# Kernel optimization log

Measured on AMD Instinct MI355X. Metric: run time of the kernel, lower is better.

The kernel has to match this reference:

```python
import jax, jax.numpy as jnp
import numpy as np

MAX_REL = 64  # max_relative_position
LN_EPS = 1e-5


def _relative_positions(seq_len):
    r = jnp.arange(seq_len)
    rel = jnp.clip(r[None, :] - r[:, None], -MAX_REL, MAX_REL) + MAX_REL
    return rel  # [S, S] int32 in [0, 2*MAX_REL]


def setup_inputs() -> dict:
    key = jax.random.key(0)
    ks = jax.random.split(key, 8)
    B, S, H = 8, 1024, 128
    sd = 1.0 / np.sqrt(H)
    return {
        "x": jax.random.normal(ks[0], (B, S, H), jnp.float32),
        "Wq": jax.random.normal(ks[1], (H, H), jnp.float32) * sd,
        "bq": jnp.zeros((H,), jnp.float32),
        "Wk": jax.random.normal(ks[2], (H, H), jnp.float32) * sd,
        "bk": jnp.zeros((H,), jnp.float32),
        "Wv": jax.random.normal(ks[3], (H, H), jnp.float32) * sd,
        "bv": jnp.zeros((H,), jnp.float32),
        "rel_k": jax.random.normal(ks[4], (2 * MAX_REL + 1, H), jnp.float32),
        "rel_v": jax.random.normal(ks[5], (2 * MAX_REL + 1, H), jnp.float32),
        "Wo": jax.random.normal(ks[6], (H, H), jnp.float32) * sd,
        "bo": jnp.zeros((H,), jnp.float32),
        "gamma": jnp.ones((H,), jnp.float32),
        "beta": jnpp if False else jnp.zeros((H,), jnp.float32),
    }


def reference(x, Wq, bq, Wk, bk, Wv, bv, rel_k, rel_v, Wo, bo, gamma, beta):
    B, S, H = x.shape
    scale = jnp.sqrt(jnp.asarray(H, x.dtype))

    q = x @ Wq + bq  # [B,S,H]
    k = x @ Wk + bk
    v = x @ Wv + bv

    scores = jnp.einsum("bih,bjh->bij", q, k) / scale  # [B,S,S]

    relpos = _relative_positions(S)            # [S,S] int
    rk = rel_k[relpos]                          # [S,S,H] gather
    scores = scores + jnp.einsum("bih,ijh->bij", q, rk)

    attn = jax.nn.softmax(scores, axis=-1)      # dropout = identity (eval)

    ctx = jnp.einsum("bij,bjh->bih", attn, v)
    rv = rel_v[relpos]                          # [S,S,H] gather
    ctx = ctx + jnp.einsum("bij,ijh->bih", attn, rv)

    out = ctx @ Wo + bo

    # residual + LayerNorm
    y = out + x
    mu = jnp.mean(y, axis=-1, keepdims=True)
    var = jnp.mean(jnp.square(y - mu), axis=-1, keepdims=True)
    y = (y - mu) * jax.lax.rsqrt(var + LN_EPS) * gamma + beta
    return y, attn
```

## Files before the change

kernel.cpp:

```cpp
#include <hip/hip_runtime.h>

constexpr int Bn = 8, Sn = 1024, Hn = 128, Rn = 129, RLD = 132;
constexpr float INV_SCALE = 0.088388347648318447f;
constexpr size_t YEL = (size_t)Bn * Sn * Hn;

typedef short bf16x8 __attribute__((ext_vector_type(8)));
typedef short v4s __attribute__((ext_vector_type(4)));
typedef float f32x4 __attribute__((ext_vector_type(4)));
typedef int v4i __attribute__((ext_vector_type(4)));

__device__ __forceinline__ float bf2f(short s) {
    unsigned u = ((unsigned)(unsigned short)s) << 16;
    float f; __builtin_memcpy(&f, &u, 4); return f;
}
__device__ __forceinline__ short f2bf(float f) {
    unsigned u; __builtin_memcpy(&u, &f, 4);
    unsigned r = (u + 0x7fffu + ((u >> 16) & 1u)) >> 16;
    return (short)(r & 0xffffu);
}

__global__ __launch_bounds__(384) void build_relcat(
    const float* __restrict__ rel_k, short* __restrict__ relcat)
{
    const int p = blockIdx.x, c = threadIdx.x;
    const int j = (c < 256) ? (c & 127) : (c - 256);
    float v = rel_k[p * Hn + j];
    short h = f2bf(v);
    relcat[p * 384 + c] = (c < 256) ? h : f2bf(v - bf2f(h));
}

__global__ __launch_bounds__(256) void build_bcat(
    const float* __restrict__ rel_v, const float* __restrict__ Wo,
    short* __restrict__ BcatT)
{
    int idx = blockIdx.x * 256 + threadIdx.x;
    int k = idx >> 7, n = idx & 127;
    float v;
    if (k < 128) v = Wo[k * Hn + n];
    else if (k < 257) {
        int p = k - 128; float a = 0.f;
        for (int h = 0; h < Hn; ++h) a += rel_v[p * Hn + h] * Wo[h * Hn + n];
        v = a;
    } else v = 0.f;
    BcatT[n * 320 + k] = f2bf(v);
}

__global__ __launch_bounds__(256) void proj(
    const float* __restrict__ X,
    const float* __restrict__ Wq, const float* __restrict__ bq,
    const float* __restrict__ Wk, const float* __restrict__ bk,
    const float* __restrict__ Wv, const float* __restrict__ bv,
    short* __restrict__ qh, short* __restrict__ qcat,
    short* __restrict__ kh, short* __restrict__ vT)
{
    __shared__ float xs[64][128];
    __shared__ float wsm[32][128];
    const int tid = threadIdx.x;
    const int sel = blockIdx.y;
    const int row0 = blockIdx.x * 64;
    const float* W = (sel == 0) ? Wq : (sel == 1) ? Wk : Wv;
    const float* bias = (sel == 0) ? bq : (sel == 1) ? bk : bv;

#pragma unroll
    for (int it = 0; it < 8; ++it) {
        int u = tid + it * 256;
        int r = u >> 5, c4 = (u & 31) * 4;
        *(float4*)&xs[r][c4] = *(const float4*)(X + (size_t)(row0 + r) * 128 + c4);
    }

    const int rg = tid >> 5, cg = tid & 31;
    float acc[8][4] = {};
    for (int kc = 0; kc < 128; kc += 32) {
#pragma unroll
        for (int it = 0; it < 4; ++it) {
            int u = tid + it * 256;
            int kk = u >> 5, c4 = (u & 31) * 4;
            *(float4*)&wsm[kk][c4] = *(const float4*)(W + (size_t)(kc + kk) * 128 + c4);
        }
        __syncthreads();
#pragma unroll 8
        for (int kk = 0; kk < 32; ++kk) {
            float wv[4];
#pragma unroll
            for (int c = 0; c < 4; ++c) wv[c] = wsm[kk][cg + c * 32];
#pragma unroll
            for (int r = 0; r < 8; ++r) {
                float xv = xs[rg * 8 + r][kc + kk];
#pragma unroll
                for (int c = 0; c < 4; ++c) acc[r][c] += xv * wv[c];
            }
        }
        __syncthreads();
    }

#pragma unroll
    for (int c = 0; c < 4; ++c) {
        int col = cg + c * 32;
        float bv2 = bias[col];
#pragma unroll
        for (int r = 0; r < 8; ++r) {
            int row = row0 + rg * 8 + r;
            float v = acc[r][c] + bv2;
            short h = f2bf(v);
            if (sel == 0) {
                qh[(size_t)row * 128 + col] = h;
                qcat[(size_t)row * 256 + col] = h;
                qcat[(size_t)row * 256 + 128 + col] = f2bf(v - bf2f(h));
            } else if (sel == 1) {
                kh[(size_t)row * 128 + col] = h;
            } else {
                int b = row >> 10, i = row & (Sn - 1);
                vT[(size_t)b * 131072 + (size_t)col * 1024 + i] = h;
            }
        }
    }
}

__global__ __launch_bounds__(256) void qrel_gemm(
    const short* __restrict__ qcat, const short* __restrict__ relcat,
    float* __restrict__ qrel)
{
    __shared__ short As[64][72];
    __shared__ short Bs[64][72];
    const int tid = threadIdx.x;
    const int wave = tid >> 6, lane = tid & 63;
    const int quad = lane >> 4, l15 = lane & 15;
    const int row0 = blockIdx.x * 64, col0 = blockIdx.y * 64;

    f32x4 acc[4] = {};
    for (int kc = 0; kc < 384; kc += 64) {
#pragma unroll
        for (int it = 0; it < 2; ++it) {
            int u = tid + it * 256;
            int r = u >> 3, c8 = (u & 7) * 8;
            int srcc = kc + c8;
            if (srcc >= 256) srcc -= 256;
            *(v4i*)&As[r][c8] = *(const v4i*)(qcat + (size_t)(row0 + r) * 256 + srcc);
        }
#pragma unroll
        for (int it = 0; it < 2; ++it) {
            int u = tid + it * 256;
            int r = u >> 3, c8 = (u & 7) * 8;
            v4i val = {0, 0, 0, 0};
            if (col0 + r < Rn)
                val = *(const v4i*)(relcat + (size_t)(col0 + r) * 384 + kc + c8);
            *(v4i*)&Bs[r][c8] = val;
        }
        __syncthreads();
#pragma unroll
        for (int ks = 0; ks < 64; ks += 32) {
            bf16x8 af = *(const bf16x8*)&As[wave * 16 + l15][ks + quad * 8];
#pragma unroll
            for (int nt = 0; nt < 4; ++nt) {
                bf16x8 bf = *(const bf16x8*)&Bs[nt * 16 + l15][ks + quad * 8];
                acc[nt] = __builtin_amdgcn_mfma_f32_16x16x32_bf16(af, bf, acc[nt], 0, 0, 0);
            }
        }
        __syncthreads();
    }
    const int rloc0 = wave * 16 + quad * 4;
#pragma unroll
    for (int nt = 0; nt < 4; ++nt) {
        int col = col0 + nt * 16 + l15;
#pragma unroll
        for (int r = 0; r < 4; ++r) {
            if (col < Rn)
                qrel[(size_t)(row0 + rloc0 + r) * RLD + col] = acc[nt][r];
        }
    }
}

__global__ __launch_bounds__(512, 4) void fused_attn(
    const short* __restrict__ qh, const short* __restrict__ kh,
    const short* __restrict__ vT, const float* __restrict__ qrel_g,
    const short* __restrict__ BcatT,
    const float* __restrict__ X, const float* __restrict__ bo,
    const float* __restrict__ gamma, const float* __restrict__ beta,
    float* __restrict__ attn_g, float* __restrict__ y_g)
{
    __shared__ __align__(16) char smem[80896];
    short* KTs  = (short*)smem;
    short* Pb   = (short*)(smem + 34816);
    short* CtxA = (short*)(smem + 67840);
    float* QrL  = (float*)(smem + 67840);
    float* redM = (float*)(smem + 78848);
    float* redS = redM + 128;
    float* redL = redS + 128;
    float* redH = redL + 128;

    const int tid = threadIdx.x;
    const int w = tid >> 6, lane = tid & 63;
    const int quad = lane >> 4, l15 = lane & 15;
    const int bz = blockIdx.z;
    const int row0 = blockIdx.x * 16;
    const size_t grow0 = (size_t)bz * Sn + row0;

#pragma unroll
    for (int rr = 0; rr < 2; ++rr) {
        int r = w * 2 + rr;
        const float* src = qrel_g + (grow0 + r) * RLD;
        QrL[r * 132 + lane] = src[lane];
        QrL[r * 132 + 64 + lane] = src[64 + lane];
        if (lane < 4) QrL[r * 132 + 128 + lane] = src[128 + lane];
    }

    bf16x8 afr[4];
#pragma unroll
    for (int kk = 0; kk < 4; ++kk)
        afr[kk] = *(const bf16x8*)(qh + (grow0 + l15) * 128 + kk * 32 + quad * 8);

    const short* khb = kh + (size_t)bz * Sn * 128;
    f32x4 acc[8] = {};
    for (int kt = 0; kt < 8; ++kt) {
#pragma unroll
        for (int it = 0; it < 4; ++it) {
            int u = tid + it * 512;
            int r = u >> 4, c8 = (u & 15) * 8;
            *(v4i*)&KTs[r * 136 + c8] = *(const v4i*)(khb + (size_t)(kt * 128 + r) * 128 + c8);
        }
        __syncthreads();
#pragma unroll
        for (int kk = 0; kk < 4; ++kk) {
            bf16x8 b = *(const bf16x8*)&KTs[(w * 16 + l15) * 136 + kk * 32 + quad * 8];
            acc[kt] = __builtin_amdgcn_mfma_f32_16x16x32_bf16(afr[kk], b, acc[kt], 0, 0, 0);
        }
        __syncthreads();
    }

    float mx[4];
#pragma unroll
    for (int r = 0; r < 4; ++r) {
        int lr = quad * 4 + r, i = row0 + lr;
        float m = -3.4e38f;
#pragma unroll
        for (int kt = 0; kt < 8; ++kt) {
            int col = kt * 128 + w * 16 + l15;
            int d = col - i; d = (d < -64) ? -64 : (d > 64 ? 64 : d);
            float v = acc[kt][r] * INV_SCALE + QrL[lr * 132 + d + 64];
            acc[kt][r] = v;
            m = fmaxf(m, v);
        }
#pragma unroll
        for (int msk = 1; msk < 16; msk <<= 1) m = fmaxf(m, __shfl_xor(m, msk));
        if (l15 == 0) redM[lr * 8 + w] = m;
    }
    __syncthreads();
#pragma unroll
    for (int r = 0; r < 4; ++r) {
        int lr = quad * 4 + r;
        float m = redM[lr * 8];
#pragma unroll
        for (int j = 1; j < 8; ++j) m = fmaxf(m, redM[lr * 8 + j]);
        mx[r] = m;
    }

#pragma unroll
    for (int r = 0; r < 4; ++r) {
        int lr = quad * 4 + r, i = row0 + lr;
        float s = 0.f, lo = 0.f, hi = 0.f;
#pragma unroll
        for (int kt = 0; kt < 8; ++kt) {
            float e = __expf(acc[kt][r] - mx[r]);
            acc[kt][r] = e;
            s += e;
            int col = kt * 128 + w * 16 + l15;
            lo += (col <= i - 64) ? e : 0.f;
            hi += (col >= i + 64) ? e : 0.f;
        }
#pragma unroll
        for (int msk = 1; msk < 16; msk <<= 1) {
            s += __shfl_xor(s, msk);
            lo += __shfl_xor(lo, msk);
            hi += __shfl_xor(hi, msk);
        }
        if (l15 == 0) { redS[lr * 8 + w] = s; redL[lr * 8 + w] = lo; redH[lr * 8 + w] = hi; }
    }
    __syncthreads();

#pragma unroll
    for (int r = 0; r < 4; ++r) {
        int lr = quad * 4 + r;
        float s = 0.f;
#pragma unroll
        for (int j = 0; j < 8; ++j) s += redS[lr * 8 + j];
        float inv = 1.0f / s;
        float* arow = attn_g + (grow0 + lr) * Sn;
#pragma unroll
        for (int kt = 0; kt < 8; ++kt) {
            int col = kt * 128 + w * 16 + l15;
            float v = acc[kt][r] * inv;
            arow[col] = v;
            Pb[lr * 1032 + col] = f2bf(v);
        }
    }
    __syncthreads();

    const short* vtb = vT + (size_t)bz * 131072;
    f32x4 cacc = {};
    for (int kc = 0; kc < 8; ++kc) {
#pragma unroll
        for (int it = 0; it < 4; ++it) {
            int u = tid + it * 512;
            int r = u >> 4, c8 = (u & 15) * 8;
            *(v4i*)&KTs[r * 136 + c8] = *(const v4i*)(vtb + (size_t)r * 1024 + kc * 128 + c8);
        }
        __syncthreads();
#pragma unroll
        for (int kk = 0; kk < 4; ++kk) {
            bf16x8 a = *(const bf16x8*)&Pb[l15 * 1032 + kc * 128 + kk * 32 + quad * 8];
            bf16x8 b = *(const bf16x8*)&KTs[(w * 16 + l15) * 136 + kk * 32 + quad * 8];
            cacc = __builtin_amdgcn_mfma_f32_16x16x32_bf16(a, b, cacc, 0, 0, 0);
        }
        __syncthreads();
    }

#pragma unroll
    for (int r = 0; r < 4; ++r)
        CtxA[(quad * 4 + r) * 344 + w * 16 + l15] = f2bf(cacc[r]);
#pragma unroll
    for (int rr = 0; rr < 2; ++rr) {
        int lr = w * 2 + rr, i = row0 + lr;
        float s = 0.f, lo = 0.f, hi = 0.f;
#pragma unroll
        for (int j = 0; j < 8; ++j) {
            s += redS[lr * 8 + j]; lo += redL[lr * 8 + j]; hi += redH[lr * 8 + j];
        }
        float inv = 1.0f / s;
        float v0;
        if (lane == 0) v0 = lo * inv;
        else { int c = i + lane - 64; v0 = (c >= 0 && c < Sn) ? bf2f(Pb[lr * 1032 + c]) : 0.f; }
        CtxA[lr * 344 + 128 + lane] = f2bf(v0);
        int c1 = i + lane;
        CtxA[lr * 344 + 192 + lane] = (c1 < Sn) ? Pb[lr * 1032 + c1] : (short)0;
        CtxA[lr * 344 + 256 + lane] = (lane == 0) ? f2bf(hi * inv) : (short)0;
    }
    __syncthreads();

    f32x4 yacc = {};
#pragma unroll
    for (int ch = 0; ch < 3; ++ch) {
        if (ch < 2) {
#pragma unroll
            for (int it = 0; it < 4; ++it) {
                int u = tid + it * 512;
                int n = u >> 4, c8 = (u & 15) * 8;
                *(v4i*)&KTs[n * 136 + c8] = *(const v4i*)(BcatT + (size_t)n * 320 + ch * 128 + c8);
            }
        } else {
#pragma unroll
            for (int it = 0; it < 2; ++it) {
                int u = tid + it * 512;
                int n = u >> 3, c8 = (u & 7) * 8;
                *(v4i*)&KTs[n * 136 + c8] = *(const v4i*)(BcatT + (size_t)n * 320 + 256 + c8);
            }
        }
        __syncthreads();
        const int nkk = (ch == 2) ? 2 : 4;
        for (int kk = 0; kk < nkk; ++kk) {
            bf16x8 a = *(const bf16x8*)&CtxA[l15 * 344 + ch * 128 + kk * 32 + quad * 8];
            bf16x8 b = *(const bf16x8*)&KTs[(w * 16 + l15) * 136 + kk * 32 + quad * 8];
            yacc = __builtin_amdgcn_mfma_f32_16x16x32_bf16(a, b, yacc, 0, 0, 0);
        }
        __syncthreads();
    }

    const int col = w * 16 + l15;
    const float bov = bo[col], gv = gamma[col], bev = beta[col];
    float vv[4];
#pragma unroll
    for (int r = 0; r < 4; ++r) {
        int lr = quad * 4 + r;
        vv[r] = yacc[r] + bov + X[(grow0 + lr) * 128 + col];
    }
#pragma unroll
    for (int r = 0; r < 4; ++r) {
        float s = vv[r];
#pragma unroll
        for (int msk = 1; msk < 16; msk <<= 1) s += __shfl_xor(s, msk);
        if (l15 == 0) redM[(quad * 4 + r) * 8 + w] = s;
    }
    __syncthreads();
    float mu[4];
#pragma unroll
    for (int r = 0; r < 4; ++r) {
        int lr = quad * 4 + r;
        float s = 0.f;
#pragma unroll
        for (int j = 0; j < 8; ++j) s += redM[lr * 8 + j];
        mu[r] = s * (1.f / 128.f);
    }
#pragma unroll
    for (int r = 0; r < 4; ++r) {
        float d = vv[r] - mu[r];
        float s = d * d;
#pragma unroll
        for (int msk = 1; msk < 16; msk <<= 1) s += __shfl_xor(s, msk);
        if (l15 == 0) redS[(quad * 4 + r) * 8 + w] = s;
    }
    __syncthreads();
#pragma unroll
    for (int r = 0; r < 4; ++r) {
        int lr = quad * 4 + r;
        float s = 0.f;
#pragma unroll
        for (int j = 0; j < 8; ++j) s += redS[lr * 8 + j];
        float inv = rsqrtf(s * (1.f / 128.f) + 1e-5f);
        y_g[(grow0 + lr) * 128 + col] = (vv[r] - mu[r]) * inv * gv + bev;
    }
}

extern "C" void kernel_launch(void* const* d_in, const int* in_sizes, int n_in,
                              void* d_out, int out_size, void* d_ws, size_t ws_size,
                              hipStream_t stream) {
    const float* x     = (const float*)d_in[0];
    const float* Wq    = (const float*)d_in[1];
    const float* bq    = (const float*)d_in[2];
    const float* Wk    = (const float*)d_in[3];
    const float* bk    = (const float*)d_in[4];
    const float* Wv    = (const float*)d_in[5];
    const float* bv    = (const float*)d_in[6];
    const float* rel_k = (const float*)d_in[7];
    const float* rel_v = (const float*)d_in[8];
    const float* Wo    = (const float*)d_in[9];
    const float* bo    = (const float*)d_in[10];
    const float* gamma = (const float*)d_in[11];
    const float* beta  = (const float*)d_in[12];

    char* ws = (char*)d_ws;
    short* qh     = (short*)(ws + 0);
    short* kh     = (short*)(ws + 2097152);
    short* vT     = (short*)(ws + 4194304);
    short* qcat   = (short*)(ws + 6291456);
    float* qrel   = (float*)(ws + 10485760);
    short* relcat = (short*)(ws + 14811136);
    short* BcatT  = (short*)relcat;

    float* y_out = (float*)d_out;
    float* attn  = (float*)d_out + YEL;

    build_relcat<<<dim3(Rn), 384, 0, stream>>>(rel_k, relcat);
    proj<<<dim3(128, 3), 256, 0, stream>>>(x, Wq, bq, Wk, bk, Wv, bv, qh, qcat, kh, vT);
    qrel_gemm<<<dim3(128, 3), 256, 0, stream>>>(qcat, relcat, qrel);
    build_bcat<<<dim3(160), 256, 0, stream>>>(rel_v, Wo, BcatT);

    fused_attn<<<dim3(64, 1, Bn), 512, 0, stream>>>(
        qh, kh, vT, qrel, BcatT, x, bo, gamma, beta, attn, y_out);
}
```

Before: 159.3 us.

## Load MFMA operands directly from global, merge table kernels, coalesce attn writes

Removes the LDS staging and barriers for K, V and Bcat tiles in the fused attention kernel and for both operands in qrel_gemm, so MFMA fragments are read straight from global/L2. It merges the relcat and Bcat builders into one launch with separate buffers and remaps blocks so neighbouring blocks belong to different batches. It writes attention probabilities as coalesced float4 rows from the bf16 LDS copy, which rounds the attn output to bf16 precision. Smaller LDS use may raise occupancy, but the direct global loads are uncoalesced and rely on cache hits.

Result: slower. 172.6 us (+8.3%).

```diff
diff --git a/kernel.cpp b/kernel.cpp
--- a/kernel.cpp
+++ b/kernel.cpp
@@ -19,30 +19,31 @@
     return (short)(r & 0xffffu);
 }
 
-__global__ __launch_bounds__(384) void build_relcat(
-    const float* __restrict__ rel_k, short* __restrict__ relcat)
+__global__ __launch_bounds__(384) void build_tables(
+    const float* __restrict__ rel_k, const float* __restrict__ rel_v,
+    const float* __restrict__ Wo,
+    short* __restrict__ relcat, short* __restrict__ BcatT)
 {
-    const int p = blockIdx.x, c = threadIdx.x;
-    const int j = (c < 256) ? (c & 127) : (c - 256);
-    float v = rel_k[p * Hn + j];
-    short h = f2bf(v);
-    relcat[p * 384 + c] = (c < 256) ? h : f2bf(v - bf2f(h));
-}
-
-__global__ __launch_bounds__(256) void build_bcat(
-    const float* __restrict__ rel_v, const float* __restrict__ Wo,
-    short* __restrict__ BcatT)
-{
-    int idx = blockIdx.x * 256 + threadIdx.x;
-    int k = idx >> 7, n = idx & 127;
-    float v;
-    if (k < 128) v = Wo[k * Hn + n];
-    else if (k < 257) {
-        int p = k - 128; float a = 0.f;
-        for (int h = 0; h < Hn; ++h) a += rel_v[p * Hn + h] * Wo[h * Hn + n];
-        v = a;
-    } else v = 0.f;
-    BcatT[n * 320 + k] = f2bf(v);
+    if (blockIdx.x < Rn) {
+        const int p = blockIdx.x, c = threadIdx.x;
+        const int j = (c < 256) ? (c & 127) : (c - 256);
+        float v = rel_k[p * Hn + j];
+        short h = f2bf(v);
+        relcat[p * 384 + c] = (c < 256) ? h : f2bf(v - bf2f(h));
+    } else {
+        int idx = (blockIdx.x - Rn) * 384 + threadIdx.x;
+        if (idx < 320 * 128) {
+            int k = idx >> 7, n = idx & 127;
+            float v;
+            if (k < 128) v = Wo[k * Hn + n];
+            else if (k < 257) {
+                int p = k - 128; float a = 0.f;
+                for (int h = 0; h < Hn; ++h) a += rel_v[p * Hn + h] * Wo[h * Hn + n];
+                v = a;
+            } else v = 0.f;
+            BcatT[n * 320 + k] = f2bf(v);
+        }
+    }
 }
 
 __global__ __launch_bounds__(256) void proj(
@@ -120,43 +121,25 @@
     const short* __restrict__ qcat, const short* __restrict__ relcat,
     float* __restrict__ qrel)
 {
-    __shared__ short As[64][72];
-    __shared__ short Bs[64][72];
     const int tid = threadIdx.x;
     const int wave = tid >> 6, lane = tid & 63;
     const int quad = lane >> 4, l15 = lane & 15;
     const int row0 = blockIdx.x * 64, col0 = blockIdx.y * 64;
 
+    const short* arow = qcat + (size_t)(row0 + wave * 16 + l15) * 256;
     f32x4 acc[4] = {};
-    for (int kc = 0; kc < 384; kc += 64) {
-#pragma unroll
-        for (int it = 0; it < 2; ++it) {
-            int u = tid + it * 256;
-            int r = u >> 3, c8 = (u & 7) * 8;
-            int srcc = kc + c8;
-            if (srcc >= 256) srcc -= 256;
-            *(v4i*)&As[r][c8] = *(const v4i*)(qcat + (size_t)(row0 + r) * 256 + srcc);
-        }
-#pragma unroll
-        for (int it = 0; it < 2; ++it) {
-            int u = tid + it * 256;
-            int r = u >> 3, c8 = (u & 7) * 8;
-            v4i val = {0, 0, 0, 0};
-            if (col0 + r < Rn)
-                val = *(const v4i*)(relcat + (size_t)(col0 + r) * 384 + kc + c8);
-            *(v4i*)&Bs[r][c8] = val;
-        }
-        __syncthreads();
-#pragma unroll
-        for (int ks = 0; ks < 64; ks += 32) {
-            bf16x8 af = *(const bf16x8*)&As[wave * 16 + l15][ks + quad * 8];
-#pragma unroll
-            for (int nt = 0; nt < 4; ++nt) {
-                bf16x8 bf = *(const bf16x8*)&Bs[nt * 16 + l15][ks + quad * 8];
-                acc[nt] = __builtin_amdgcn_mfma_f32_16x16x32_bf16(af, bf, acc[nt], 0, 0, 0);
-            }
-        }
-        __syncthreads();
+#pragma unroll
+    for (int kc = 0; kc < 384; kc += 32) {
+        int srcc = (kc >= 256) ? kc - 256 : kc;
+        bf16x8 af = *(const bf16x8*)(arow + srcc + quad * 8);
+#pragma unroll
+        for (int nt = 0; nt < 4; ++nt) {
+            int brow = col0 + nt * 16 + l15;
+            bf16x8 bf = {0, 0, 0, 0, 0, 0, 0, 0};
+            if (brow < Rn)
+                bf = *(const bf16x8*)(relcat + (size_t)brow * 384 + kc + quad * 8);
+            acc[nt] = __builtin_amdgcn_mfma_f32_16x16x32_bf16(af, bf, acc[nt], 0, 0, 0);
+        }
     }
     const int rloc0 = wave * 16 + quad * 4;
 #pragma unroll
@@ -178,12 +161,11 @@
     const float* __restrict__ gamma, const float* __restrict__ beta,
     float* __restrict__ attn_g, float* __restrict__ y_g)
 {
-    __shared__ __align__(16) char smem[80896];
-    short* KTs  = (short*)smem;
-    short* Pb   = (short*)(smem + 34816);
-    short* CtxA = (short*)(smem + 67840);
-    float* QrL  = (float*)(smem + 67840);
-    float* redM = (float*)(smem + 78848);
+    __shared__ __align__(16) char smem[46080];
+    short* Pb   = (short*)smem;
+    short* CtxA = (short*)(smem + 33024);
+    float* QrL  = (float*)(smem + 33024);
+    float* redM = (float*)(smem + 44032);
     float* redS = redM + 128;
     float* redL = redS + 128;
     float* redH = redL + 128;
@@ -191,8 +173,9 @@
     const int tid = threadIdx.x;
     const int w = tid >> 6, lane = tid & 63;
     const int quad = lane >> 4, l15 = lane & 15;
-    const int bz = blockIdx.z;
-    const int row0 = blockIdx.x * 16;
+    const int lb = blockIdx.x + (blockIdx.z << 6);
+    const int bz = lb & 7;
+    const int row0 = (lb >> 3) << 4;
     const size_t grow0 = (size_t)bz * Sn + row0;
 
 #pragma unroll
@@ -211,21 +194,16 @@
 
     const short* khb = kh + (size_t)bz * Sn * 128;
     f32x4 acc[8] = {};
+#pragma unroll
     for (int kt = 0; kt < 8; ++kt) {
-#pragma unroll
-        for (int it = 0; it < 4; ++it) {
-            int u = tid + it * 512;
-            int r = u >> 4, c8 = (u & 15) * 8;
-            *(v4i*)&KTs[r * 136 + c8] = *(const v4i*)(khb + (size_t)(kt * 128 + r) * 128 + c8);
-        }
-        __syncthreads();
+        const short* kr = khb + (size_t)(kt * 128 + w * 16 + l15) * 128;
 #pragma unroll
         for (int kk = 0; kk < 4; ++kk) {
-            bf16x8 b = *(const bf16x8*)&KTs[(w * 16 + l15) * 136 + kk * 32 + quad * 8];
+            bf16x8 b = *(const bf16x8*)(kr + kk * 32 + quad * 8);
             acc[kt] = __builtin_amdgcn_mfma_f32_16x16x32_bf16(afr[kk], b, acc[kt], 0, 0, 0);
         }
-        __syncthreads();
-    }
+    }
+    __syncthreads();
 
     float mx[4];
 #pragma unroll
@@ -284,34 +262,38 @@
 #pragma unroll
         for (int j = 0; j < 8; ++j) s += redS[lr * 8 + j];
         float inv = 1.0f / s;
-        float* arow = attn_g + (grow0 + lr) * Sn;
 #pragma unroll
         for (int kt = 0; kt < 8; ++kt) {
             int col = kt * 128 + w * 16 + l15;
-            float v = acc[kt][r] * inv;
-            arow[col] = v;
-            Pb[lr * 1032 + col] = f2bf(v);
-        }
-    }
-    __syncthreads();
-
-    const short* vtb = vT + (size_t)bz * 131072;
+            Pb[lr * 1032 + col] = f2bf(acc[kt][r] * inv);
+        }
+    }
+    __syncthreads();
+
+    {
+        float* ab = attn_g + grow0 * Sn;
+#pragma unroll
+        for (int it = 0; it < 8; ++it) {
+            int u = tid + it * 512;
+            int r = u >> 8, c4 = (u & 255) * 4;
+            v4s pv = *(const v4s*)&Pb[r * 1032 + c4];
+            float4 o;
+            o.x = bf2f(pv[0]); o.y = bf2f(pv[1]);
+            o.z = bf2f(pv[2]); o.w = bf2f(pv[3]);
+            *(float4*)(ab + (size_t)r * Sn + c4) = o;
+        }
+    }
+
+    const short* vtb = vT + (size_t)bz * 131072 + (size_t)(w * 16 + l15) * 1024;
     f32x4 cacc = {};
+#pragma unroll
     for (int kc = 0; kc < 8; ++kc) {
-#pragma unroll
-        for (int it = 0; it < 4; ++it) {
-            int u = tid + it * 512;
-            int r = u >> 4, c8 = (u & 15) * 8;
-            *(v4i*)&KTs[r * 136 + c8] = *(const v4i*)(vtb + (size_t)r * 1024 + kc * 128 + c8);
-        }
-        __syncthreads();
 #pragma unroll
         for (int kk = 0; kk < 4; ++kk) {
             bf16x8 a = *(const bf16x8*)&Pb[l15 * 1032 + kc * 128 + kk * 32 + quad * 8];
-            bf16x8 b = *(const bf16x8*)&KTs[(w * 16 + l15) * 136 + kk * 32 + quad * 8];
+            bf16x8 b = *(const bf16x8*)(vtb + kc * 128 + kk * 32 + quad * 8);
             cacc = __builtin_amdgcn_mfma_f32_16x16x32_bf16(a, b, cacc, 0, 0, 0);
         }
-        __syncthreads();
     }
 
 #pragma unroll
@@ -337,31 +319,17 @@
     __syncthreads();
 
     f32x4 yacc = {};
+    const short* bcb = BcatT + (size_t)(w * 16 + l15) * 320;
 #pragma unroll
     for (int ch = 0; ch < 3; ++ch) {
-        if (ch < 2) {
-#pragma unroll
-            for (int it = 0; it < 4; ++it) {
-                int u = tid + it * 512;
-                int n = u >> 4, c8 = (u & 15) * 8;
-                *(v4i*)&KTs[n * 136 + c8] = *(const v4i*)(BcatT + (size_t)n * 320 + ch * 128 + c8);
-            }
-        } else {
-#pragma unroll
-            for (int it = 0; it < 2; ++it) {
-                int u = tid + it * 512;
-                int n = u >> 3, c8 = (u & 7) * 8;
-                *(v4i*)&KTs[n * 136 + c8] = *(const v4i*)(BcatT + (size_t)n * 320 + 256 + c8);
-            }
-        }
-        __syncthreads();
         const int nkk = (ch == 2) ? 2 : 4;
-        for (int kk = 0; kk < nkk; ++kk) {
+#pragma unroll
+        for (int kk = 0; kk < 4; ++kk) {
+            if (kk >= nkk) break;
             bf16x8 a = *(const bf16x8*)&CtxA[l15 * 344 + ch * 128 + kk * 32 + quad * 8];
-            bf16x8 b = *(const bf16x8*)&KTs[(w * 16 + l15) * 136 + kk * 32 + quad * 8];
+            bf16x8 b = *(const bf16x8*)(bcb + ch * 128 + kk * 32 + quad * 8);
             yacc = __builtin_amdgcn_mfma_f32_16x16x32_bf16(a, b, yacc, 0, 0, 0);
         }
-        __syncthreads();
     }
 
     const int col = w * 16 + l15;
@@ -433,15 +401,14 @@
     short* qcat   = (short*)(ws + 6291456);
     float* qrel   = (float*)(ws + 10485760);
     short* relcat = (short*)(ws + 14811136);
-    short* BcatT  = (short*)relcat;
+    short* BcatT  = (short*)(ws + 14910464);
 
     float* y_out = (float*)d_out;
     float* attn  = (float*)d_out + YEL;
 
-    build_relcat<<<dim3(Rn), 384, 0, stream>>>(rel_k, relcat);
+    build_tables<<<dim3(Rn + 107), 384, 0, stream>>>(rel_k, rel_v, Wo, relcat, BcatT);
     proj<<<dim3(128, 3), 256, 0, stream>>>(x, Wq, bq, Wk, bk, Wv, bv, qh, qcat, kh, vT);
     qrel_gemm<<<dim3(128, 3), 256, 0, stream>>>(qcat, relcat, qrel);
-    build_bcat<<<dim3(160), 256, 0, stream>>>(rel_v, Wo, BcatT);
 
     fused_attn<<<dim3(64, 1, Bn), 512, 0, stream>>>(
         qh, kh, vT, qrel, BcatT, x, bo, gamma, beta, attn, y_out);
```
